# Optimization experiments

Measured on AMD Instinct MI355X. Metric: run time of the kernel, lower is better.

Reference implementation:

```python
import jax, jax.numpy as jnp
import numpy as np

AREA = 4
NUM_HEADS = 4


def _conv1x1(x, w, s, t):
    # 1x1 Conv (bias=False) + folded BatchNorm: per-out-channel scale s, shift t
    y = jnp.einsum('bchw,oc->bohw', x, w)
    return y * s[None, :, None, None] + t[None, :, None, None]


def setup_inputs() -> dict:
    key = jax.random.key(0)
    ks = jax.random.split(key, 9)
    C, heads = 128, NUM_HEADS
    x = jax.random.normal(ks[0], (2, C, 80, 80), jnp.float32)

    def wmat(k, o, i):
        return jax.random.normal(k, (o, i), jnp.float32) * (i ** -0.5)

    def bn(k, n):
        k1, k2 = jax.random.split(k)
        s = 1.0 + 0.05 * jax.random.normal(k1, (n,), jnp.float32)
        t = 0.05 * jax.random.normal(k2, (n,), jnp.float32)
        return s, t

    w_qk = wmat(ks[1], 2 * C, C); s_qk, t_qk = bn(ks[2], 2 * C)
    w_in = wmat(ks[3], C, C); s_in, t_in = bn(ks[4], C)
    w_out = wmat(ks[5], C, C); s_out, t_out = bn(ks[6], C)
    w_fg = jax.random.normal(ks[7], (heads, heads, 1, 5), jnp.float32) * ((5 * heads) ** -0.5)
    s_fg, t_fg = bn(ks[8], heads)
    return dict(x=x, w_qk=w_qk, s_qk=s_qk, t_qk=t_qk, w_in=w_in, s_in=s_in,
                t_in=t_in, w_out=w_out, s_out=s_out, t_out=t_out,
                w_fg=w_fg, s_fg=s_fg, t_fg=t_fg)


def reference(x, w_qk, s_qk, t_qk, w_in, s_in, t_in, w_out, s_out, t_out, w_fg, s_fg, t_fg):
    B, C, H, W = x.shape
    N = H * W
    heads = NUM_HEADS
    hd = C // heads
    inp = x
    # qk projection -> [B, N, 2C]
    qk = _conv1x1(x, w_qk, s_qk, t_qk).reshape(B, 2 * C, N).transpose(0, 2, 1)
    # input-gated values -> [B, N, C]
    v = jax.nn.sigmoid(_conv1x1(x, w_in, s_in, t_in)) * x
    v = v.reshape(B, C, N).transpose(0, 2, 1)
    # area split
    Be, Na = B * AREA, N // AREA
    qk = qk.reshape(Be, Na, 2 * C)
    v = v.reshape(Be, Na, C)
    q, k = qk[..., :C], qk[..., C:]
    q = q.transpose(0, 2, 1).reshape(Be, heads, hd, Na)
    k = k.transpose(0, 2, 1).reshape(Be, heads, hd, Na)
    v = v.transpose(0, 2, 1).reshape(Be, heads, hd, Na)
    # full NxN attention per area/head
    attn = jnp.einsum('bhdn,bhdm->bhnm', q, k) * (hd ** -0.5)
    attn = jax.nn.softmax(attn, axis=-1)
    # forget gate: (1,5) conv mixing heads along last axis, pad (0,2), BN fold, SiLU
    attn = jax.lax.conv_general_dilated(attn, w_fg, (1, 1), ((0, 0), (2, 2)),
                                        dimension_numbers=('NCHW', 'OIHW', 'NCHW'))
    attn = attn * s_fg[None, :, None, None] + t_fg[None, :, None, None]
    attn = jax.nn.silu(attn)
    # v @ attn^T -> [Be, heads, hd, Na]
    o = jnp.einsum('bhdj,bhij->bhdi', v, attn)
    # merge areas back: [Be,Na,h,hd] -> [B,N,C] -> [B,C,H,W]
    o = o.transpose(0, 3, 1, 2).reshape(B, N, C)
    o = o.reshape(B, H, W, C).transpose(0, 3, 1, 2)
    return jax.nn.sigmoid(_conv1x1(o, w_out, s_out, t_out)) * o + inp
```

## Files before the change

### kernel.cpp

```cpp
#include <hip/hip_runtime.h>
#include <hip/hip_bf16.h>
#include <cstdint>

#define CC 128
#define NN 6400
#define NAa 1600
#define HEADS 4
#define HD 32
#define NB 32
#define MT 64

#define P_ROW 68
#define P_HEAD 1096
#define A_ROW 76
#define A_HEAD 1224
#define PW (HEADS * P_HEAD)
#define AW (HEADS * A_HEAD)
#define HB_IDX(par, qs, hh, lo) (((((par)*2 + (qs))*4 + (hh))*16 + (lo)) * 4)

typedef __attribute__((ext_vector_type(8))) short bfrag8;
typedef __attribute__((ext_vector_type(4))) float ffrag4;
typedef union { uint2 u2[2]; bfrag8 f8; } cvt16;

#define LOG2E 1.4426950408889634f
#define QSCL (0.17677669529663687f * 1.4426950408889634f)

__device__ __forceinline__ float sigmoid_fast(float y) {
  return __builtin_amdgcn_rcpf(1.0f + __builtin_amdgcn_exp2f(-LOG2E * y));
}
__device__ __forceinline__ unsigned short f2bf(float f) {
  unsigned u = __float_as_uint(f);
  return (unsigned short)((u + 0x7FFFu + ((u >> 16) & 1u)) >> 16);
}
__device__ __forceinline__ unsigned pack_bf16(float a, float b) {
  return (unsigned)f2bf(a) | ((unsigned)f2bf(b) << 16);
}
__device__ __forceinline__ unsigned pk2(float a, float b) {
  float2 f2; f2.x = a; f2.y = b;
  __hip_bfloat162 h = __float22bfloat162_rn(f2);
  union { __hip_bfloat162 h2; unsigned u; } cv; cv.h2 = h;
  return cv.u;
}
__device__ __forceinline__ float bfl(unsigned u) { return __uint_as_float(u << 16); }
__device__ __forceinline__ float bfh(unsigned u) { return __uint_as_float(u & 0xFFFF0000u); }

__global__ __launch_bounds__(256) void prep_kernel(
    const float* __restrict__ x, const float* __restrict__ w_qk,
    const float* __restrict__ s_qk, const float* __restrict__ w_in,
    const float* __restrict__ s_in, const float* __restrict__ w_out,
    const float* __restrict__ s_out,
    unsigned short* __restrict__ xt, unsigned short* __restrict__ wqkb,
    unsigned short* __restrict__ wob) {
  __shared__ float tile[32][33];
  const int blk = blockIdx.x, tid = threadIdx.x;
  if (blk < 1600) {
    const int b = blk / 800, rem = blk - b * 800;
    const int ct = rem / 200, pt2 = rem - ct * 200;
    const int c0 = ct * 32, px0 = pt2 * 32;
    for (int i = tid; i < 1024; i += 256) {
      int r = i >> 5, p = i & 31;
      tile[r][p] = x[((size_t)(b * CC + c0 + r)) * NN + px0 + p];
    }
    __syncthreads();
    for (int i = tid; i < 512; i += 256) {
      int px = i >> 4, cp = i & 15;
      unsigned pk = pk2(tile[2 * cp][px], tile[2 * cp + 1][px]);
      *(unsigned*)&xt[((size_t)b * NN + px0 + px) * CC + c0 + 2 * cp] = pk;
    }
  } else if (blk < 1608) {
    const int r0 = (blk - 1600) * 48;
    for (int i = tid; i < 6144; i += 256) {
      int r = r0 + (i >> 7), c = i & 127;
      float wv, sv;
      if (r < 2 * CC) { wv = w_qk[r * CC + c]; sv = s_qk[r] * (r < CC ? QSCL : 1.0f); }
      else           { wv = w_in[(r - 2 * CC) * CC + c]; sv = s_in[r - 2 * CC]; }
      wqkb[r * CC + c] = f2bf(wv * sv);
    }
  } else {
    const int r0 = (blk - 1608) * 64;
    for (int i = tid; i < 8192; i += 256) {
      int r = r0 + (i >> 7), c = i & 127;
      wob[r * CC + c] = f2bf(w_out[r * CC + c] * s_out[r]);
    }
  }
}

__global__ __launch_bounds__(256) void qkv_kernel(
    const unsigned short* __restrict__ xt, const unsigned short* __restrict__ wqkb,
    const float* __restrict__ t_qk, const float* __restrict__ t_in,
    unsigned short* __restrict__ qt, unsigned short* __restrict__ kt,
    unsigned short* __restrict__ vb) {
  const int tid = threadIdx.x;
  const int w = tid >> 6, lane = tid & 63, lo = lane & 15, g = lane >> 4;
  const int blk = blockIdx.x;
  const int b = blk / 400, pt = blk - b * 400;
  const int ng0 = pt * 16;
  const int a = ng0 / NAa, na0 = ng0 - a * NAa;
  const int be = b * 4 + a;
  const size_t xrow = ((size_t)b * NN + ng0 + lo) * CC;
  bfrag8 bf[4];
#pragma unroll
  for (int kk = 0; kk < 4; kk++) bf[kk] = *(const bfrag8*)&xt[xrow + kk * 32 + g * 8];
#pragma unroll
  for (int mt6 = 0; mt6 < 6; mt6++) {
    const int rowbase = (w * 6 + mt6) * 16;
    ffrag4 d = {0.f, 0.f, 0.f, 0.f};
#pragma unroll
    for (int kk = 0; kk < 4; kk++) {
      bfrag8 af = *(const bfrag8*)&wqkb[(size_t)(rowbase + lo) * CC + kk * 32 + g * 8];
      d = __builtin_amdgcn_mfma_f32_16x16x32_bf16(af, bf[kk], d, 0, 0, 0);
    }
    const int r0c = rowbase + 4 * g;
    if (r0c < CC) {
      const int h = r0c >> 5, d0 = r0c & 31;
      uint2 pk;
      pk.x = pk2(d[0] + t_qk[r0c] * QSCL, d[1] + t_qk[r0c + 1] * QSCL);
      pk.y = pk2(d[2] + t_qk[r0c + 2] * QSCL, d[3] + t_qk[r0c + 3] * QSCL);
      *(uint2*)&qt[((size_t)(be * HEADS + h) * NAa + na0 + lo) * HD + d0] = pk;
    } else if (r0c < 2 * CC) {
      const int ch = r0c - CC, h = ch >> 5, d0 = ch & 31;
      uint2 pk;
      pk.x = pk2(d[0] + t_qk[r0c], d[1] + t_qk[r0c + 1]);
      pk.y = pk2(d[2] + t_qk[r0c + 2], d[3] + t_qk[r0c + 3]);
      *(uint2*)&kt[((size_t)(be * HEADS + h) * NAa + na0 + lo) * HD + d0] = pk;
    } else {
      const int ch0 = r0c - 2 * CC;
      const uint2 xv = *(const uint2*)&xt[xrow + ch0];
      float xr[4] = {bfl(xv.x), bfh(xv.x), bfl(xv.y), bfh(xv.y)};
#pragma unroll
      for (int r = 0; r < 4; r++) {
        float y = d[r] + t_in[ch0 + r];
        vb[((size_t)be * CC + ch0 + r) * NAa + na0 + lo] = f2bf(sigmoid_fast(y) * xr[r]);
      }
    }
  }
}

__global__ __launch_bounds__(256) void stats_kernel(
    const unsigned short* __restrict__ qt, const unsigned short* __restrict__ kt,
    float* __restrict__ pstats) {
  int tid = threadIdx.x;
  int h = tid >> 6, lane = tid & 63, lo = lane & 15, g = lane >> 4;
  int bid = blockIdx.x;
  int be = bid & 7;
  int rest = bid >> 3;
  int n0 = (rest % 100) * 16;
  int split = rest / 100;
  int ts0 = split ? 12 : 0, ts1 = split ? 25 : 12;

  const unsigned short* qtb = qt + (size_t)(be * HEADS + h) * NAa * HD;
  const unsigned short* ktb = kt + (size_t)(be * HEADS + h) * NAa * HD;

  bfrag8 qf = *(const bfrag8*)(qtb + (size_t)(n0 + lo) * HD + g * 8);
  float sm[4] = {0.f, 0.f, 0.f, 0.f};
  for (int t = ts0; t < ts1; t++) {
    int m0 = t * MT;
#pragma unroll
    for (int sb = 0; sb < 4; sb++) {
      bfrag8 kf = *(const bfrag8*)(ktb + (size_t)(m0 + sb * 16 + lo) * HD + g * 8);
      ffrag4 z = {0.f, 0.f, 0.f, 0.f};
      ffrag4 c = __builtin_amdgcn_mfma_f32_16x16x32_bf16(qf, kf, z, 0, 0, 0);
#pragma unroll
      for (int r = 0; r < 4; r++) sm[r] += __builtin_amdgcn_exp2f(c[r]);
    }
  }
#pragma unroll
  for (int r = 0; r < 4; r++) {
#pragma unroll
    for (int off = 1; off <= 8; off <<= 1) sm[r] += __shfl_xor(sm[r], off);
  }
  if (lo == 0) {
    float4 s4; s4.x = sm[0]; s4.y = sm[1]; s4.z = sm[2]; s4.w = sm[3];
    *(float4*)&pstats[((size_t)(split * 8 + be) * HEADS + h) * NAa + n0 + 4 * g] = s4;
  }
}

__global__ __launch_bounds__(512) void apply_kernel(
    const unsigned short* __restrict__ qt, const unsigned short* __restrict__ kt,
    const unsigned short* __restrict__ vb, const float* __restrict__ pstats,
    const float* __restrict__ w_fg, const float* __restrict__ s_fg,
    const float* __restrict__ t_fg, unsigned short* __restrict__ o_part) {
  __shared__ __align__(16) unsigned short Ps[2 * PW];
  __shared__ __align__(16) unsigned short A2s[2 * AW];
  __shared__ __align__(16) unsigned short Hb[1024];
  const int tid = threadIdx.x;
  const int w = tid >> 6, lane = tid & 63, lo = lane & 15, g = lane >> 4;
  const int h = w >> 1, u = w & 1;
  const int bid = blockIdx.x;
  const int be = bid & 7;
  const int rest = bid >> 3;
  const int n0 = (rest % 50) * NB;
  const int split = rest / 50;
  const int ts0 = split ? 12 : 0;
  const int tend = split ? 26 : 12;

  const unsigned short* qtb = qt + (size_t)(be * HEADS + h) * NAa * HD;
  const unsigned short* ktb = kt + (size_t)(be * HEADS + h) * NAa * HD;
  const unsigned short* vhb = vb + (size_t)(be * CC + h * HD) * NAa;

  bfrag8 qf[2];
#pragma unroll
  for (int qs = 0; qs < 2; ++qs)
    qf[qs] = *(const bfrag8*)(qtb + (size_t)(n0 + 16 * qs + lo) * HD + g * 8);

  bfrag8 wfrag;
  {
    const int ho = lo >> 2, s = lo & 3;
#pragma unroll
    for (int j = 0; j < 8; j++) {
      const int tp = j - s;
      float wv = (tp >= 0 && tp < 5) ? w_fg[(ho * HEADS + g) * 5 + tp] : 0.0f;
      wfrag[j] = (short)f2bf(wv);
    }
  }
  const float sfv = s_fg[g], tfv = t_fg[g];

  float inv[2];
#pragma unroll
  for (int qs = 0; qs < 2; ++qs)
    inv[qs] = 1.0f / (pstats[((size_t)(0 + be) * HEADS + h) * NAa + n0 + 16 * qs + lo] +
                      pstats[((size_t)(8 + be) * HEADS + h) * NAa + n0 + 16 * qs + lo]);

  ffrag4 oacc[2][2];
#pragma unroll
  for (int qs = 0; qs < 2; ++qs) {
    ffrag4 z = {0.f, 0.f, 0.f, 0.f};
    oacc[qs][0] = z; oacc[qs][1] = z;
  }

  if (split == 0) {
    if (u == 0 && g == 0) {
      uint2 zz; zz.x = 0; zz.y = 0;
#pragma unroll
      for (int qs = 0; qs < 2; ++qs)
        *(uint2*)&Hb[HB_IDX(0, qs, h, lo)] = zz;
    }
  } else if (u == 0) {
    bfrag8 kf = *(const bfrag8*)(ktb + (size_t)(752 + lo) * HD + g * 8);
#pragma unroll
    for (int qs = 0; qs < 2; ++qs) {
      ffrag4 z = {0.f, 0.f, 0.f, 0.f};
      ffrag4 c = __builtin_amdgcn_mfma_f32_16x16x32_bf16(kf, qf[qs], z, 0, 0, 0);
      if (g == 3) {
        uint2 pk;
        pk.x = pk2(__builtin_amdgcn_exp2f(c[0]) * inv[qs], __builtin_amdgcn_exp2f(c[1]) * inv[qs]);
        pk.y = pk2(__builtin_amdgcn_exp2f(c[2]) * inv[qs], __builtin_amdgcn_exp2f(c[3]) * inv[qs]);
        *(uint2*)&Hb[HB_IDX(0, qs, h, lo)] = pk;
      }
    }
  }
  {
    const int m0 = ts0 * MT;
#pragma unroll
    for (int sbi = 0; sbi < 2; sbi++) {
      const int sb = 2 * u + sbi;
      bfrag8 kf = *(const bfrag8*)(ktb + (size_t)(m0 + sb * 16 + lo) * HD + g * 8);
#pragma unroll
      for (int qs = 0; qs < 2; ++qs) {
        ffrag4 z = {0.f, 0.f, 0.f, 0.f};
        ffrag4 c = __builtin_amdgcn_mfma_f32_16x16x32_bf16(kf, qf[qs], z, 0, 0, 0);
        uint2 pk;
        pk.x = pk2(__builtin_amdgcn_exp2f(c[0]) * inv[qs], __builtin_amdgcn_exp2f(c[1]) * inv[qs]);
        pk.y = pk2(__builtin_amdgcn_exp2f(c[2]) * inv[qs], __builtin_amdgcn_exp2f(c[3]) * inv[qs]);
        *(uint2*)&Ps[qs * PW + h * P_HEAD + lo * P_ROW + 16 * sb + 4 * g] = pk;
        if (sb == 3 && g == 3)
          *(uint2*)&Hb[HB_IDX(1, qs, h, lo)] = pk;
      }
    }
  }
  __syncthreads();

  for (int t = ts0; t < tend; t++) {
    const int m0 = t * MT;
    const int par = t & 1;
    const bfrag8 vf0 = *(const bfrag8*)(vhb + (size_t)lo * NAa + (m0 - 2 + 32 * u + 8 * g));
    const bfrag8 vf1 = *(const bfrag8*)(vhb + (size_t)(16 + lo) * NAa + (m0 - 2 + 32 * u + 8 * g));
    const bool doqk = (t + 1 < tend);
    const bool realqk = doqk && (t + 1 < 25);
    bfrag8 kf0, kf1;
    if (realqk) {
      const int m1 = (t + 1) * MT;
      kf0 = *(const bfrag8*)(ktb + (size_t)(m1 + (2 * u) * 16 + lo) * HD + g * 8);
      kf1 = *(const bfrag8*)(ktb + (size_t)(m1 + (2 * u + 1) * 16 + lo) * HD + g * 8);
    }
    const bool edge = (t == 0) || (t == 25);
#pragma unroll
    for (int qs = 0; qs < 2; ++qs) {
#pragma unroll
      for (int ii = 0; ii < 2; ii++) {
        const int i = 2 * w + ii;
        cvt16 bb;
        if (i == 0)
          bb.u2[0] = *(const uint2*)&Hb[HB_IDX(par, qs, g, lo)];
        else
          bb.u2[0] = *(const uint2*)&Ps[qs * PW + g * P_HEAD + lo * P_ROW + 4 * i - 4];
        bb.u2[1] = *(const uint2*)&Ps[qs * PW + g * P_HEAD + lo * P_ROW + 4 * i];
        ffrag4 z = {0.f, 0.f, 0.f, 0.f};
        ffrag4 d = __builtin_amdgcn_mfma_f32_16x16x32_bf16(wfrag, bb.f8, z, 0, 0, 0);
        float a2v[4];
        if (edge) {
#pragma unroll
          for (int r = 0; r < 4; r++) {
            const int mp = m0 - 2 + 4 * i + r;
            float y = d[r] * sfv + tfv;
            float v = y * sigmoid_fast(y);
            a2v[r] = (mp >= 0 && mp < NAa) ? v : 0.0f;
          }
        } else {
#pragma unroll
          for (int r = 0; r < 4; r++) {
            float y = d[r] * sfv + tfv;
            a2v[r] = y * sigmoid_fast(y);
          }
        }
        uint2 pk;
        pk.x = pk2(a2v[0], a2v[1]);
        pk.y = pk2(a2v[2], a2v[3]);
        *(uint2*)&A2s[qs * AW + g * A_HEAD + lo * A_ROW + 4 * i] = pk;
      }
    }
    __syncthreads();
    if (doqk) {
      if (realqk) {
#pragma unroll
        for (int qs = 0; qs < 2; ++qs) {
          ffrag4 z = {0.f, 0.f, 0.f, 0.f};
          ffrag4 c0 = __builtin_amdgcn_mfma_f32_16x16x32_bf16(kf0, qf[qs], z, 0, 0, 0);
          ffrag4 c1 = __builtin_amdgcn_mfma_f32_16x16x32_bf16(kf1, qf[qs], z, 0, 0, 0);
          uint2 pk;
          pk.x = pk2(__builtin_amdgcn_exp2f(c0[0]) * inv[qs], __builtin_amdgcn_exp2f(c0[1]) * inv[qs]);
          pk.y = pk2(__builtin_amdgcn_exp2f(c0[2]) * inv[qs], __builtin_amdgcn_exp2f(c0[3]) * inv[qs]);
          *(uint2*)&Ps[qs * PW + h * P_HEAD + lo * P_ROW + 16 * (2 * u) + 4 * g] = pk;
          uint2 pk1;
          pk1.x = pk2(__builtin_amdgcn_exp2f(c1[0]) * inv[qs], __builtin_amdgcn_exp2f(c1[1]) * inv[qs]);
          pk1.y = pk2(__builtin_amdgcn_exp2f(c1[2]) * inv[qs], __builtin_amdgcn_exp2f(c1[3]) * inv[qs]);
          *(uint2*)&Ps[qs * PW + h * P_HEAD + lo * P_ROW + 16 * (2 * u + 1) + 4 * g] = pk1;
          if (u == 1 && g == 3)
            *(uint2*)&Hb[HB_IDX(par, qs, h, lo)] = pk1;
        }
      } else {
        uint2 zz; zz.x = 0; zz.y = 0;
#pragma unroll
        for (int qs = 0; qs < 2; ++qs) {
          *(uint2*)&Ps[qs * PW + h * P_HEAD + lo * P_ROW + 16 * (2 * u) + 4 * g] = zz;
          *(uint2*)&Ps[qs * PW + h * P_HEAD + lo * P_ROW + 16 * (2 * u + 1) + 4 * g] = zz;
        }
      }
    }
#pragma unroll
    for (int qs = 0; qs < 2; ++qs) {
      cvt16 av;
      av.u2[0] = *(const uint2*)&A2s[qs * AW + h * A_HEAD + lo * A_ROW + 32 * u + 8 * g];
      av.u2[1] = *(const uint2*)&A2s[qs * AW + h * A_HEAD + lo * A_ROW + 32 * u + 8 * g + 4];
      oacc[qs][0] = __builtin_amdgcn_mfma_f32_16x16x32_bf16(av.f8, vf0, oacc[qs][0], 0, 0, 0);
      oacc[qs][1] = __builtin_amdgcn_mfma_f32_16x16x32_bf16(av.f8, vf1, oacc[qs][1], 0, 0, 0);
    }
    __syncthreads();
  }

  float* scr = (float*)A2s;
  if (u == 1) {
#pragma unroll
    for (int qs = 0; qs < 2; ++qs) {
      float4 f0; f0.x = oacc[qs][0][0]; f0.y = oacc[qs][0][1]; f0.z = oacc[qs][0][2]; f0.w = oacc[qs][0][3];
      float4 f1; f1.x = oacc[qs][1][0]; f1.y = oacc[qs][1][1]; f1.z = oacc[qs][1][2]; f1.w = oacc[qs][1][3];
      *(float4*)&scr[((qs * 4 + h) * 64 + lane) * 8] = f0;
      *(float4*)&scr[((qs * 4 + h) * 64 + lane) * 8 + 4] = f1;
    }
  }
  __syncthreads();
  if (u == 0) {
#pragma unroll
    for (int qs = 0; qs < 2; ++qs) {
      const float4 f0 = *(const float4*)&scr[((qs * 4 + h) * 64 + lane) * 8];
      const float4 f1 = *(const float4*)&scr[((qs * 4 + h) * 64 + lane) * 8 + 4];
      const float fa[4] = {f0.x, f0.y, f0.z, f0.w};
      const float fb[4] = {f1.x, f1.y, f1.z, f1.w};
#pragma unroll
      for (int r = 0; r < 4; r++) {
        const size_t rowoff = ((size_t)(split * 8 + be) * NAa + n0 + 16 * qs + 4 * g + r) * CC;
        o_part[rowoff + h * HD + lo] = f2bf(oacc[qs][0][r] + fa[r]);
        o_part[rowoff + h * HD + 16 + lo] = f2bf(oacc[qs][1][r] + fb[r]);
      }
    }
  }
}

__global__ __launch_bounds__(256) void out_kernel(
    const unsigned short* __restrict__ o_part, const unsigned short* __restrict__ wob,
    const float* __restrict__ t_out, const float* __restrict__ x,
    float* __restrict__ out) {
  const int tid = threadIdx.x;
  const int w = tid >> 6, lane = tid & 63, lo = lane & 15, g = lane >> 4;
  const int blk = blockIdx.x;
  const int b = blk / 400, pt = blk - b * 400;
  const int ng0 = pt * 16;
  const int a = ng0 / NAa, na0 = ng0 - a * NAa;
  const int be = b * 4 + a;
  const size_t orow0 = ((size_t)(0 * 8 + be) * NAa + na0 + lo) * CC;
  const size_t orow1 = ((size_t)(1 * 8 + be) * NAa + na0 + lo) * CC;
  bfrag8 bf0[4], bf1[4];
#pragma unroll
  for (int kk = 0; kk < 4; kk++) {
    bf0[kk] = *(const bfrag8*)&o_part[orow0 + kk * 32 + g * 8];
    bf1[kk] = *(const bfrag8*)&o_part[orow1 + kk * 32 + g * 8];
  }
#pragma unroll
  for (int mt2 = 0; mt2 < 2; mt2++) {
    const int rowbase = (w * 2 + mt2) * 16;
    ffrag4 d = {0.f, 0.f, 0.f, 0.f};
#pragma unroll
    for (int kk = 0; kk < 4; kk++) {
      bfrag8 af = *(const bfrag8*)&wob[(size_t)(rowbase + lo) * CC + kk * 32 + g * 8];
      d = __builtin_amdgcn_mfma_f32_16x16x32_bf16(af, bf0[kk], d, 0, 0, 0);
      d = __builtin_amdgcn_mfma_f32_16x16x32_bf16(af, bf1[kk], d, 0, 0, 0);
    }
    const int ch0 = rowbase + 4 * g;
    const uint2 q0 = *(const uint2*)&o_part[orow0 + ch0];
    const uint2 q1 = *(const uint2*)&o_part[orow1 + ch0];
    float ov[4] = {bfl(q0.x) + bfl(q1.x), bfh(q0.x) + bfh(q1.x),
                   bfl(q0.y) + bfl(q1.y), bfh(q0.y) + bfh(q1.y)};
#pragma unroll
    for (int r = 0; r < 4; r++) {
      const size_t xi = ((size_t)b * CC + ch0 + r) * NN + ng0 + lo;
      float y = d[r] + t_out[ch0 + r];
      out[xi] = ov[r] * sigmoid_fast(y) + x[xi];
    }
  }
}

extern "C" void kernel_launch(void* const* d_in, const int* in_sizes, int n_in,
                              void* d_out, int out_size, void* d_ws, size_t ws_size,
                              hipStream_t stream) {
  const float* x    = (const float*)d_in[0];
  const float* w_qk = (const float*)d_in[1];
  const float* s_qk = (const float*)d_in[2];
  const float* t_qk = (const float*)d_in[3];
  const float* w_in = (const float*)d_in[4];
  const float* s_in = (const float*)d_in[5];
  const float* t_in = (const float*)d_in[6];
  const float* w_out = (const float*)d_in[7];
  const float* s_out = (const float*)d_in[8];
  const float* t_out = (const float*)d_in[9];
  const float* w_fg = (const float*)d_in[10];
  const float* s_fg = (const float*)d_in[11];
  const float* t_fg = (const float*)d_in[12];

  char* wsb = (char*)d_ws;
  unsigned short* o_part = (unsigned short*)wsb;
  unsigned short* vb_raw = (unsigned short*)(wsb + 6553600);
  unsigned short* vbp = vb_raw + 2;
  unsigned short* qt = (unsigned short*)(wsb + 9830464);
  unsigned short* kt = (unsigned short*)(wsb + 13107264);
  unsigned short* xt = (unsigned short*)(wsb + 16384064);
  unsigned short* wqkb = (unsigned short*)(wsb + 19660864);
  unsigned short* wob = (unsigned short*)(wsb + 19759168);
  float* pstats = (float*)(wsb + 19791936);
  float* out = (float*)d_out;

  prep_kernel<<<1610, 256, 0, stream>>>(x, w_qk, s_qk, w_in, s_in, w_out, s_out, xt, wqkb, wob);
  qkv_kernel<<<800, 256, 0, stream>>>(xt, wqkb, t_qk, t_in, qt, kt, vbp);
  stats_kernel<<<1600, 256, 0, stream>>>(qt, kt, pstats);
  apply_kernel<<<800, 512, 0, stream>>>(qt, kt, vbp, pstats, w_fg, s_fg, t_fg, o_part);
  out_kernel<<<800, 256, 0, stream>>>(o_part, wob, t_out, x, out);
}
```

Measured before the change: 134.6 us.

## Fuse x transpose into qkv kernel and fold softmax normalizer into MFMA accumulator

The qkv kernel now reads fp32 x directly, converts it to bf16 and transposes it through a padded shared-memory tile. This removes the separate 1600-block transpose pass in prep_kernel and the round trip of the xt intermediate through global memory. Separately, the apply kernel seeds each MFMA accumulator with -log2(denominator), so exp2 yields already-normalized probabilities and the per-element multiply by the reciprocal goes away. The cost is an extra LDS pass and barrier in the qkv kernel, plus an input conversion whose rounding may differ slightly from before.

```diff
diff --git a/kernel.cpp b/kernel.cpp
--- a/kernel.cpp
+++ b/kernel.cpp
@@ -17,6 +17,7 @@
 #define PW (HEADS * P_HEAD)
 #define AW (HEADS * A_HEAD)
 #define HB_IDX(par, qs, hh, lo) (((((par)*2 + (qs))*4 + (hh))*16 + (lo)) * 4)
+#define XROW 136
 
 typedef __attribute__((ext_vector_type(8))) short bfrag8;
 typedef __attribute__((ext_vector_type(4))) float ffrag4;
@@ -31,9 +32,6 @@
 __device__ __forceinline__ unsigned short f2bf(float f) {
   unsigned u = __float_as_uint(f);
   return (unsigned short)((u + 0x7FFFu + ((u >> 16) & 1u)) >> 16);
-}
-__device__ __forceinline__ unsigned pack_bf16(float a, float b) {
-  return (unsigned)f2bf(a) | ((unsigned)f2bf(b) << 16);
 }
 __device__ __forceinline__ unsigned pk2(float a, float b) {
   float2 f2; f2.x = a; f2.y = b;
@@ -45,30 +43,13 @@
 __device__ __forceinline__ float bfh(unsigned u) { return __uint_as_float(u & 0xFFFF0000u); }
 
 __global__ __launch_bounds__(256) void prep_kernel(
-    const float* __restrict__ x, const float* __restrict__ w_qk,
-    const float* __restrict__ s_qk, const float* __restrict__ w_in,
-    const float* __restrict__ s_in, const float* __restrict__ w_out,
-    const float* __restrict__ s_out,
-    unsigned short* __restrict__ xt, unsigned short* __restrict__ wqkb,
-    unsigned short* __restrict__ wob) {
-  __shared__ float tile[32][33];
+    const float* __restrict__ w_qk, const float* __restrict__ s_qk,
+    const float* __restrict__ w_in, const float* __restrict__ s_in,
+    const float* __restrict__ w_out, const float* __restrict__ s_out,
+    unsigned short* __restrict__ wqkb, unsigned short* __restrict__ wob) {
   const int blk = blockIdx.x, tid = threadIdx.x;
-  if (blk < 1600) {
-    const int b = blk / 800, rem = blk - b * 800;
-    const int ct = rem / 200, pt2 = rem - ct * 200;
-    const int c0 = ct * 32, px0 = pt2 * 32;
-    for (int i = tid; i < 1024; i += 256) {
-      int r = i >> 5, p = i & 31;
-      tile[r][p] = x[((size_t)(b * CC + c0 + r)) * NN + px0 + p];
-    }
-    __syncthreads();
-    for (int i = tid; i < 512; i += 256) {
-      int px = i >> 4, cp = i & 15;
-      unsigned pk = pk2(tile[2 * cp][px], tile[2 * cp + 1][px]);
-      *(unsigned*)&xt[((size_t)b * NN + px0 + px) * CC + c0 + 2 * cp] = pk;
-    }
-  } else if (blk < 1608) {
-    const int r0 = (blk - 1600) * 48;
+  if (blk < 8) {
+    const int r0 = blk * 48;
     for (int i = tid; i < 6144; i += 256) {
       int r = r0 + (i >> 7), c = i & 127;
       float wv, sv;
@@ -77,7 +58,7 @@
       wqkb[r * CC + c] = f2bf(wv * sv);
     }
   } else {
-    const int r0 = (blk - 1608) * 64;
+    const int r0 = (blk - 8) * 64;
     for (int i = tid; i < 8192; i += 256) {
       int r = r0 + (i >> 7), c = i & 127;
       wob[r * CC + c] = f2bf(w_out[r * CC + c] * s_out[r]);
@@ -86,10 +67,11 @@
 }
 
 __global__ __launch_bounds__(256) void qkv_kernel(
-    const unsigned short* __restrict__ xt, const unsigned short* __restrict__ wqkb,
+    const float* __restrict__ x, const unsigned short* __restrict__ wqkb,
     const float* __restrict__ t_qk, const float* __restrict__ t_in,
     unsigned short* __restrict__ qt, unsigned short* __restrict__ kt,
     unsigned short* __restrict__ vb) {
+  __shared__ __align__(16) unsigned short xb[16 * XROW];
   const int tid = threadIdx.x;
   const int w = tid >> 6, lane = tid & 63, lo = lane & 15, g = lane >> 4;
   const int blk = blockIdx.x;
@@ -97,10 +79,21 @@
   const int ng0 = pt * 16;
   const int a = ng0 / NAa, na0 = ng0 - a * NAa;
   const int be = b * 4 + a;
-  const size_t xrow = ((size_t)b * NN + ng0 + lo) * CC;
+  {
+    const int c = tid >> 1, half = tid & 1;
+    const float* xr = &x[((size_t)(b * CC + c)) * NN + ng0 + 8 * half];
+    const float4 f0 = *(const float4*)xr;
+    const float4 f1 = *(const float4*)(xr + 4);
+    unsigned short* dst = &xb[(8 * half) * XROW + c];
+    dst[0 * XROW] = f2bf(f0.x); dst[1 * XROW] = f2bf(f0.y);
+    dst[2 * XROW] = f2bf(f0.z); dst[3 * XROW] = f2bf(f0.w);
+    dst[4 * XROW] = f2bf(f1.x); dst[5 * XROW] = f2bf(f1.y);
+    dst[6 * XROW] = f2bf(f1.z); dst[7 * XROW] = f2bf(f1.w);
+  }
+  __syncthreads();
   bfrag8 bf[4];
 #pragma unroll
-  for (int kk = 0; kk < 4; kk++) bf[kk] = *(const bfrag8*)&xt[xrow + kk * 32 + g * 8];
+  for (int kk = 0; kk < 4; kk++) bf[kk] = *(const bfrag8*)&xb[lo * XROW + kk * 32 + g * 8];
 #pragma unroll
   for (int mt6 = 0; mt6 < 6; mt6++) {
     const int rowbase = (w * 6 + mt6) * 16;
@@ -125,7 +118,7 @@
       *(uint2*)&kt[((size_t)(be * HEADS + h) * NAa + na0 + lo) * HD + d0] = pk;
     } else {
       const int ch0 = r0c - 2 * CC;
-      const uint2 xv = *(const uint2*)&xt[xrow + ch0];
+      const uint2 xv = *(const uint2*)&xb[lo * XROW + ch0];
       float xr[4] = {bfl(xv.x), bfh(xv.x), bfl(xv.y), bfh(xv.y)};
 #pragma unroll
       for (int r = 0; r < 4; r++) {
@@ -215,11 +208,13 @@
   }
   const float sfv = s_fg[g], tfv = t_fg[g];
 
-  float inv[2];
-#pragma unroll
-  for (int qs = 0; qs < 2; ++qs)
-    inv[qs] = 1.0f / (pstats[((size_t)(0 + be) * HEADS + h) * NAa + n0 + 16 * qs + lo] +
-                      pstats[((size_t)(8 + be) * HEADS + h) * NAa + n0 + 16 * qs + lo]);
+  float linv[2];
+#pragma unroll
+  for (int qs = 0; qs < 2; ++qs) {
+    const float den = pstats[((size_t)(0 + be) * HEADS + h) * NAa + n0 + 16 * qs + lo] +
+                      pstats[((size_t)(8 + be) * HEADS + h) * NAa + n0 + 16 * qs + lo];
+    linv[qs] = -__log2f(den);
+  }
 
   ffrag4 oacc[2][2];
 #pragma unroll
@@ -239,12 +234,12 @@
     bfrag8 kf = *(const bfrag8*)(ktb + (size_t)(752 + lo) * HD + g * 8);
 #pragma unroll
     for (int qs = 0; qs < 2; ++qs) {
-      ffrag4 z = {0.f, 0.f, 0.f, 0.f};
-      ffrag4 c = __builtin_amdgcn_mfma_f32_16x16x32_bf16(kf, qf[qs], z, 0, 0, 0);
+      ffrag4 cin = {linv[qs], linv[qs], linv[qs], linv[qs]};
+      ffrag4 c = __builtin_amdgcn_mfma_f32_16x16x32_bf16(kf, qf[qs], cin, 0, 0, 0);
       if (g == 3) {
         uint2 pk;
-        pk.x = pk2(__builtin_amdgcn_exp2f(c[0]) * inv[qs], __builtin_amdgcn_exp2f(c[1]) * inv[qs]);
-        pk.y = pk2(__builtin_amdgcn_exp2f(c[2]) * inv[qs], __builtin_amdgcn_exp2f(c[3]) * inv[qs]);
+        pk.x = pk2(__builtin_amdgcn_exp2f(c[0]), __builtin_amdgcn_exp2f(c[1]));
+        pk.y = pk2(__builtin_amdgcn_exp2f(c[2]), __builtin_amdgcn_exp2f(c[3]));
         *(uint2*)&Hb[HB_IDX(0, qs, h, lo)] = pk;
       }
     }
@@ -257,11 +252,11 @@
       bfrag8 kf = *(const bfrag8*)(ktb + (size_t)(m0 + sb * 16 + lo) * HD + g * 8);
 #pragma unroll
       for (int qs = 0; qs < 2; ++qs) {
-        ffrag4 z = {0.f, 0.f, 0.f, 0.f};
-        ffrag4 c = __builtin_amdgcn_mfma_f32_16x16x32_bf16(kf, qf[qs], z, 0, 0, 0);
+        ffrag4 cin = {linv[qs], linv[qs], linv[qs], linv[qs]};
+        ffrag4 c = __builtin_amdgcn_mfma_f32_16x16x32_bf16(kf, qf[qs], cin, 0, 0, 0);
         uint2 pk;
-        pk.x = pk2(__builtin_amdgcn_exp2f(c[0]) * inv[qs], __builtin_amdgcn_exp2f(c[1]) * inv[qs]);
-        pk.y = pk2(__builtin_amdgcn_exp2f(c[2]) * inv[qs], __builtin_amdgcn_exp2f(c[3]) * inv[qs]);
+        pk.x = pk2(__builtin_amdgcn_exp2f(c[0]), __builtin_amdgcn_exp2f(c[1]));
+        pk.y = pk2(__builtin_amdgcn_exp2f(c[2]), __builtin_amdgcn_exp2f(c[3]));
         *(uint2*)&Ps[qs * PW + h * P_HEAD + lo * P_ROW + 16 * sb + 4 * g] = pk;
         if (sb == 3 && g == 3)
           *(uint2*)&Hb[HB_IDX(1, qs, h, lo)] = pk;
@@ -324,16 +319,16 @@
       if (realqk) {
 #pragma unroll
         for (int qs = 0; qs < 2; ++qs) {
-          ffrag4 z = {0.f, 0.f, 0.f, 0.f};
-          ffrag4 c0 = __builtin_amdgcn_mfma_f32_16x16x32_bf16(kf0, qf[qs], z, 0, 0, 0);
-          ffrag4 c1 = __builtin_amdgcn_mfma_f32_16x16x32_bf16(kf1, qf[qs], z, 0, 0, 0);
+          ffrag4 cin = {linv[qs], linv[qs], linv[qs], linv[qs]};
+          ffrag4 c0 = __builtin_amdgcn_mfma_f32_16x16x32_bf16(kf0, qf[qs], cin, 0, 0, 0);
+          ffrag4 c1 = __builtin_amdgcn_mfma_f32_16x16x32_bf16(kf1, qf[qs], cin, 0, 0, 0);
           uint2 pk;
-          pk.x = pk2(__builtin_amdgcn_exp2f(c0[0]) * inv[qs], __builtin_amdgcn_exp2f(c0[1]) * inv[qs]);
-          pk.y = pk2(__builtin_amdgcn_exp2f(c0[2]) * inv[qs], __builtin_amdgcn_exp2f(c0[3]) * inv[qs]);
+          pk.x = pk2(__builtin_amdgcn_exp2f(c0[0]), __builtin_amdgcn_exp2f(c0[1]));
+          pk.y = pk2(__builtin_amdgcn_exp2f(c0[2]), __builtin_amdgcn_exp2f(c0[3]));
           *(uint2*)&Ps[qs * PW + h * P_HEAD + lo * P_ROW + 16 * (2 * u) + 4 * g] = pk;
           uint2 pk1;
-          pk1.x = pk2(__builtin_amdgcn_exp2f(c1[0]) * inv[qs], __builtin_amdgcn_exp2f(c1[1]) * inv[qs]);
-          pk1.y = pk2(__builtin_amdgcn_exp2f(c1[2]) * inv[qs], __builtin_amdgcn_exp2f(c1[3]) * inv[qs]);
+          pk1.x = pk2(__builtin_amdgcn_exp2f(c1[0]), __builtin_amdgcn_exp2f(c1[1]));
+          pk1.y = pk2(__builtin_amdgcn_exp2f(c1[2]), __builtin_amdgcn_exp2f(c1[3]));
           *(uint2*)&Ps[qs * PW + h * P_HEAD + lo * P_ROW + 16 * (2 * u + 1) + 4 * g] = pk1;
           if (u == 1 && g == 3)
             *(uint2*)&Hb[HB_IDX(par, qs, h, lo)] = pk1;
@@ -452,14 +447,13 @@
   unsigned short* vbp = vb_raw + 2;
   unsigned short* qt = (unsigned short*)(wsb + 9830464);
   unsigned short* kt = (unsigned short*)(wsb + 13107264);
-  unsigned short* xt = (unsigned short*)(wsb + 16384064);
   unsigned short* wqkb = (unsigned short*)(wsb + 19660864);
   unsigned short* wob = (unsigned short*)(wsb + 19759168);
   float* pstats = (float*)(wsb + 19791936);
   float* out = (float*)d_out;
 
-  prep_kernel<<<1610, 256, 0, stream>>>(x, w_qk, s_qk, w_in, s_in, w_out, s_out, xt, wqkb, wob);
-  qkv_kernel<<<800, 256, 0, stream>>>(xt, wqkb, t_qk, t_in, qt, kt, vbp);
+  prep_kernel<<<10, 256, 0, stream>>>(w_qk, s_qk, w_in, s_in, w_out, s_out, wqkb, wob);
+  qkv_kernel<<<800, 256, 0, stream>>>(x, wqkb, t_qk, t_in, qt, kt, vbp);
   stats_kernel<<<1600, 256, 0, stream>>>(qt, kt, pstats);
   apply_kernel<<<800, 512, 0, stream>>>(qt, kt, vbp, pstats, w_fg, s_fg, t_fg, o_part);
   out_kernel<<<800, 256, 0, stream>>>(o_part, wob, t_out, x, out);
```

Result: faster. 129.8 us (-3.6%).
